# Performance work log

Measured on AMD Instinct MI355X. Metric: run time of the kernel, lower is better.

Reference implementation:

```python
import jax, jax.numpy as jnp
import numpy as np

B, T, TAU = 4, 512, 512
D_MODEL = 1024  # in_dim == out_dim (required: pos embedding dim out_dim feeds pos_proj with in_size=in_dim)
H, D = 16, 64
LN_EPS = 1e-5


def rel_shift(x):
    # x: [B, T, L, H] -> Transformer-XL relative shift
    b, t, l, h = x.shape
    x = jnp.pad(x, ((0, 0), (0, 0), (1, 0), (0, 0)))  # pad j-dim front
    x = x.reshape(b, l + 1, t, h)[:, 1:, :, :]
    return x.reshape(b, t, l, h)


def setup_inputs() -> dict:
    key = jax.random.key(0)
    ks = jax.random.split(key, 7)
    s = 0.02
    return {
        "inputs": jax.random.normal(ks[0], (B, T, D_MODEL), jnp.float32),
        "memory": jax.random.normal(ks[1], (B, TAU, D_MODEL), jnp.float32),
        "w_qkv": jax.random.normal(ks[2], (3 * H * D, D_MODEL), jnp.float32) * s,
        "w_pos": jax.random.normal(ks[3], (H * D, D_MODEL), jnp.float32) * s,
        "w_out": jax.random.normal(ks[4], (D_MODEL, H * D), jnp.float32) * s,
        "uvar": jax.random.normal(ks[5], (H, D), jnp.float32) * s,
        "vvar": jax.random.normal(ks[6], (H, D), jnp.float32) * s,
        "ln_gamma": jnp.ones((D_MODEL,), jnp.float32),
        "ln_beta": jnp.zeros((D_MODEL,), jnp.float32),
    }


def reference(inputs, memory, w_qkv, w_pos, w_out, uvar, vvar, ln_gamma, ln_beta):
    b, t, din = inputs.shape
    tau = memory.shape[1]
    L = tau + t
    h, d = uvar.shape

    x = jnp.concatenate([jax.lax.stop_gradient(memory), inputs], axis=1)  # [B,L,Din]
    # input layernorm
    mu = jnp.mean(x, axis=-1, keepdims=True)
    var = jnp.mean((x - mu) ** 2, axis=-1, keepdims=True)
    x = (x - mu) / jnp.sqrt(var + LN_EPS) * ln_gamma + ln_beta

    qkv = x @ w_qkv.T  # [B,L,3HD]
    q, k, v = jnp.split(qkv, 3, axis=-1)
    q = q[:, -t:].reshape(b, t, h, d)
    k = k.reshape(b, L, h, d)
    v = v.reshape(b, L, h, d)

    # sinusoidal relative position embedding, dim = out_dim (= din here)
    inv_freq = 1.0 / (10000.0 ** (jnp.arange(0, din, 2, dtype=jnp.float32) / din))
    pos = jnp.arange(L - 1, -1, -1, dtype=jnp.float32)
    sin_in = pos[:, None] * inv_freq[None, :]                 # [L, din/2]
    phi = jnp.concatenate([jnp.sin(sin_in), jnp.cos(sin_in)], axis=-1)  # [L, din]
    R = (phi @ w_pos.T).reshape(L, h, d)

    score = jnp.einsum('bihd,bjhd->bijh', q + uvar, k)        # content score
    pos_score = jnp.einsum('bihd,jhd->bijh', q + vvar, R)     # position score
    score = (score + rel_shift(pos_score)) / (d ** 0.5)       # [B,T,L,H]

    # causal mask: query i attends to j <= tau + i
    mask = (jnp.arange(L)[None, :] <= (tau + jnp.arange(t))[:, None]).astype(score.dtype)
    mask = mask[None, :, :, None]
    masked = score * mask + 1e30 * (mask - 1.0)
    w = jax.nn.softmax(masked, axis=2)

    out = jnp.einsum('bijh,bjhd->bihd', w, v).reshape(b, t, h * d)
    return out @ w_out.T
```

## Files before the change

### kernel.cpp

```cpp
#include <hip/hip_runtime.h>
#include <math.h>

#define B_   4
#define T_   512
#define TAU_ 512
#define L_   1024
#define DM_  1024
#define H_   16
#define D_   64

typedef short  s16x8 __attribute__((ext_vector_type(8)));
typedef ushort u16x4 __attribute__((ext_vector_type(4)));
typedef float  f32x4 __attribute__((ext_vector_type(4)));

__device__ __forceinline__ ushort f2bf(float x) {
  uint u = __float_as_uint(x);
  u += 0x7fffu + ((u >> 16) & 1u);
  return (ushort)(u >> 16);
}
__device__ __forceinline__ float bf2f(ushort u) {
  return __uint_as_float(((uint)u) << 16);
}
__device__ __forceinline__ int sw64(int row, int col) {
  return row * 64 + (col ^ ((row & 7) << 3));
}

__global__ __launch_bounds__(256) void prep_kernel(
    const float* __restrict__ inp, const float* __restrict__ mem,
    const float* __restrict__ gamma, const float* __restrict__ beta,
    ushort* __restrict__ xn, ushort* __restrict__ phi,
    const float* __restrict__ wq, ushort* __restrict__ wqb,
    const float* __restrict__ wp, ushort* __restrict__ wpb,
    const float* __restrict__ wo, ushort* __restrict__ wob) {
  int blk = blockIdx.x;
  int t = threadIdx.x;
  if (blk < 4096) {
    int row = blk;
    int b = row >> 10, l = row & 1023;
    const float* src = (l < TAU_)
        ? mem + ((size_t)b * TAU_ + l) * DM_
        : inp + ((size_t)b * T_ + (l - TAU_)) * DM_;
    float4 v = *(const float4*)(src + t * 4);
    float s  = v.x + v.y + v.z + v.w;
    float s2 = v.x * v.x + v.y * v.y + v.z * v.z + v.w * v.w;
#pragma unroll
    for (int off = 32; off > 0; off >>= 1) {
      s  += __shfl_down(s, off);
      s2 += __shfl_down(s2, off);
    }
    __shared__ float red[8];
    __shared__ float stat[2];
    int wid = t >> 6;
    if ((t & 63) == 0) { red[wid * 2] = s; red[wid * 2 + 1] = s2; }
    __syncthreads();
    if (t == 0) {
      float ts  = red[0] + red[2] + red[4] + red[6];
      float ts2 = red[1] + red[3] + red[5] + red[7];
      float mu  = ts * (1.0f / DM_);
      float var = ts2 * (1.0f / DM_) - mu * mu;
      stat[0] = mu;
      stat[1] = 1.0f / sqrtf(var + 1e-5f);
    }
    __syncthreads();
    float mu = stat[0], rstd = stat[1];
    float4 g  = *(const float4*)(gamma + t * 4);
    float4 be = *(const float4*)(beta  + t * 4);
    u16x4 o;
    o[0] = f2bf((v.x - mu) * rstd * g.x + be.x);
    o[1] = f2bf((v.y - mu) * rstd * g.y + be.y);
    o[2] = f2bf((v.z - mu) * rstd * g.z + be.z);
    o[3] = f2bf((v.w - mu) * rstd * g.w + be.w);
    *(u16x4*)(xn + (size_t)row * DM_ + t * 4) = o;
  } else if (blk < 8192) {
    int idx = (blk - 4096) * 256 + t;
    int m = idx >> 10, c = idx & 1023;
    float p = (float)(1023 - m);
    int cc = (c < 512) ? c : c - 512;
    float invf = __expf(-((float)(2 * cc) * (1.0f / 1024.0f)) * 9.210340371976184f);
    float a = p * invf;
    phi[idx] = f2bf((c < 512) ? sinf(a) : cosf(a));
  } else {
    int i = (blk - 8192) * 256 + t;
    const float* src; ushort* dst; int off;
    if (i < 786432)       { src = wq; dst = wqb; off = i; }
    else if (i < 1048576) { src = wp; dst = wpb; off = i - 786432; }
    else                  { src = wo; dst = wob; off = i - 1048576; }
    float4 v = *(const float4*)(src + (size_t)off * 4);
    u16x4 o = { f2bf(v.x), f2bf(v.y), f2bf(v.z), f2bf(v.w) };
    *(u16x4*)(dst + (size_t)off * 4) = o;
  }
}

template <typename CT>
__device__ __forceinline__ void gemm_nt_body(
    const ushort* __restrict__ A, const ushort* __restrict__ B,
    CT* __restrict__ C, int M, int N, int K, int bx, int by) {
  __shared__ __attribute__((aligned(16))) ushort As[128 * 64];
  __shared__ __attribute__((aligned(16))) ushort Bs[128 * 64];
  int t = threadIdx.x;
  int w = t >> 6, lane = t & 63, g = lane >> 4, low = lane & 15;
  int wr = w >> 1, wc = w & 1;
  int m0 = by * 128, n0 = bx * 128;
  f32x4 acc[4][4] = {};

  for (int kt = 0; kt < K; kt += 64) {
    __syncthreads();
#pragma unroll
    for (int q = 0; q < 4; ++q) {
      int c = t + q * 256;
      int row = c >> 3;
      int gslot = (c & 7) ^ (row & 7);
      const ushort* ga = A + (size_t)(m0 + row) * K + kt + gslot * 8;
      const ushort* gb = B + (size_t)(n0 + row) * K + kt + gslot * 8;
      __builtin_amdgcn_global_load_lds(
          (const __attribute__((address_space(1))) void*)ga,
          (__attribute__((address_space(3))) void*)&As[(q * 256 + w * 64) * 8],
          16, 0, 0);
      __builtin_amdgcn_global_load_lds(
          (const __attribute__((address_space(1))) void*)gb,
          (__attribute__((address_space(3))) void*)&Bs[(q * 256 + w * 64) * 8],
          16, 0, 0);
    }
    __syncthreads();

#pragma unroll
    for (int kc = 0; kc < 2; ++kc) {
      s16x8 af[4], bfr[4];
#pragma unroll
      for (int mi = 0; mi < 4; ++mi) {
        int row = wr * 64 + mi * 16 + low;
        af[mi] = *(const s16x8*)&As[row * 64 + (((4 * kc + g) ^ (row & 7)) * 8)];
      }
#pragma unroll
      for (int ni = 0; ni < 4; ++ni) {
        int col = wc * 64 + ni * 16 + low;
        bfr[ni] = *(const s16x8*)&Bs[col * 64 + (((4 * kc + g) ^ (col & 7)) * 8)];
      }
#pragma unroll
      for (int mi = 0; mi < 4; ++mi)
#pragma unroll
        for (int ni = 0; ni < 4; ++ni)
          acc[mi][ni] = __builtin_amdgcn_mfma_f32_16x16x32_bf16(
              af[mi], bfr[ni], acc[mi][ni], 0, 0, 0);
    }
  }
#pragma unroll
  for (int mi = 0; mi < 4; ++mi)
#pragma unroll
    for (int ni = 0; ni < 4; ++ni)
#pragma unroll
      for (int r = 0; r < 4; ++r) {
        int m = m0 + wr * 64 + mi * 16 + 4 * g + r;
        int n = n0 + wc * 64 + ni * 16 + low;
        if constexpr (sizeof(CT) == 2)
          C[(size_t)m * N + n] = f2bf(acc[mi][ni][r]);
        else
          C[(size_t)m * N + n] = acc[mi][ni][r];
      }
}

template <typename CT>
__device__ __forceinline__ void gemm_nt_body_n64(
    const ushort* __restrict__ A, const ushort* __restrict__ B,
    CT* __restrict__ C, int M, int N, int K, int bx, int by) {
  __shared__ __attribute__((aligned(16))) ushort As[128 * 64];
  __shared__ __attribute__((aligned(16))) ushort Bs[64 * 64];
  int t = threadIdx.x;
  int w = t >> 6, lane = t & 63, g = lane >> 4, low = lane & 15;
  int wr = w >> 1, wc = w & 1;
  int m0 = by * 128, n0 = bx * 64;
  f32x4 acc[4][2] = {};

  for (int kt = 0; kt < K; kt += 64) {
    __syncthreads();
#pragma unroll
    for (int q = 0; q < 4; ++q) {
      int c = t + q * 256;
      int row = c >> 3;
      int gslot = (c & 7) ^ (row & 7);
      const ushort* ga = A + (size_t)(m0 + row) * K + kt + gslot * 8;
      __builtin_amdgcn_global_load_lds(
          (const __attribute__((address_space(1))) void*)ga,
          (__attribute__((address_space(3))) void*)&As[(q * 256 + w * 64) * 8],
          16, 0, 0);
    }
#pragma unroll
    for (int q = 0; q < 2; ++q) {
      int c = t + q * 256;
      int row = c >> 3;
      int gslot = (c & 7) ^ (row & 7);
      const ushort* gb = B + (size_t)(n0 + row) * K + kt + gslot * 8;
      __builtin_amdgcn_global_load_lds(
          (const __attribute__((address_space(1))) void*)gb,
          (__attribute__((address_space(3))) void*)&Bs[(q * 256 + w * 64) * 8],
          16, 0, 0);
    }
    __syncthreads();

#pragma unroll
    for (int kc = 0; kc < 2; ++kc) {
      s16x8 af[4], bfr[2];
#pragma unroll
      for (int mi = 0; mi < 4; ++mi) {
        int row = wr * 64 + mi * 16 + low;
        af[mi] = *(const s16x8*)&As[row * 64 + (((4 * kc + g) ^ (row & 7)) * 8)];
      }
#pragma unroll
      for (int ni = 0; ni < 2; ++ni) {
        int col = wc * 32 + ni * 16 + low;
        bfr[ni] = *(const s16x8*)&Bs[col * 64 + (((4 * kc + g) ^ (col & 7)) * 8)];
      }
#pragma unroll
      for (int mi = 0; mi < 4; ++mi)
#pragma unroll
        for (int ni = 0; ni < 2; ++ni)
          acc[mi][ni] = __builtin_amdgcn_mfma_f32_16x16x32_bf16(
              af[mi], bfr[ni], acc[mi][ni], 0, 0, 0);
    }
  }
#pragma unroll
  for (int mi = 0; mi < 4; ++mi)
#pragma unroll
    for (int ni = 0; ni < 2; ++ni)
#pragma unroll
      for (int r = 0; r < 4; ++r) {
        int m = m0 + wr * 64 + mi * 16 + 4 * g + r;
        int n = n0 + wc * 32 + ni * 16 + low;
        if constexpr (sizeof(CT) == 2)
          C[(size_t)m * N + n] = f2bf(acc[mi][ni][r]);
        else
          C[(size_t)m * N + n] = acc[mi][ni][r];
      }
}

__global__ __launch_bounds__(256) void qkv_r_gemm(
    const ushort* __restrict__ xnb, const ushort* __restrict__ wqb,
    ushort* __restrict__ qkvB,
    const ushort* __restrict__ phib, const ushort* __restrict__ wpb,
    ushort* __restrict__ RmB) {
  int orig = blockIdx.x;
  int id = (orig & 7) * 104 + (orig >> 3);
  if (id < 768)
    gemm_nt_body<ushort>(xnb, wqb, qkvB, 4096, 3072, 1024, id % 24, id / 24);
  else {
    id -= 768;
    gemm_nt_body<ushort>(phib, wpb, RmB, 1024, 1024, 1024, id % 8, id / 8);
  }
}

__global__ __launch_bounds__(256) void out_gemm(
    const ushort* __restrict__ attnb, const ushort* __restrict__ wob,
    float* __restrict__ out) {
  int orig = blockIdx.x;
  int id = (orig & 7) * 32 + (orig >> 3);
  gemm_nt_body_n64<float>(attnb, wob, out, 2048, 1024, 1024, id % 16, id / 16);
}

__global__ __launch_bounds__(256) void attn_mfma_kernel(
    const ushort* __restrict__ qkv, const ushort* __restrict__ Rm,
    const float* __restrict__ uvar, const float* __restrict__ vvar,
    ushort* __restrict__ attn) {
  __shared__ __attribute__((aligned(16))) ushort Ks[2][64 * 64];
  __shared__ __attribute__((aligned(16))) ushort Vt[2][64 * 64];
  __shared__ __attribute__((aligned(16))) ushort Rs[2][128 * 64];
  __shared__ __attribute__((aligned(16))) ushort Pp[4][16 * 64];

  int t   = threadIdx.x;
  int w   = t >> 6;
  int lw  = t & 63;
  int g   = lw >> 4;
  int low = lw & 15;

  int bid = blockIdx.x;
  int h   = (bid >> 3) & 15;
  int b   = bid >> 7;
  int bi  = (b >= 2) ? (7 - (bid & 7)) : (bid & 7);
  int i0  = bi * 64;
  int lb_w = 48 - 16 * w;

  auto stage_kr = [&](int buf, int tl) {
    int j0s = tl * 64;
#pragma unroll
    for (int q = 0; q < 2; ++q) {
      int c = t + q * 256;
      int row = c >> 3;
      int sl = (c & 7) ^ (row & 7);
      const ushort* srck = qkv + (size_t)(b * L_ + j0s + row) * 3072 +
                           1024 + h * 64 + sl * 8;
      __builtin_amdgcn_global_load_lds(
          (const __attribute__((address_space(1))) void*)srck,
          (__attribute__((address_space(3))) void*)&Ks[buf][(q * 256 + w * 64) * 8],
          16, 0, 0);
    }
    int mb = j0s + 448 - i0;
#pragma unroll
    for (int q = 0; q < 4; ++q) {
      int c = t + q * 256;
      int row = c >> 3;
      int m = mb + row; m = (m > 1023) ? 1023 : m;
      int sl = (c & 7) ^ (row & 7);
      const ushort* srcr = Rm + (size_t)m * 1024 + h * 64 + sl * 8;
      __builtin_amdgcn_global_load_lds(
          (const __attribute__((address_space(1))) void*)srcr,
          (__attribute__((address_space(3))) void*)&Rs[buf][(q * 256 + w * 64) * 8],
          16, 0, 0);
    }
  };

  int vj  = t & 63;
  int vd0 = (t >> 6) * 8;
  float4 vreg[2];
  auto vload = [&](int tl) {
    const ushort* p = qkv + (size_t)(b * L_ + tl * 64 + vj) * 3072 + 2048 + h * 64;
    vreg[0] = *(const float4*)(p + vd0);
    vreg[1] = *(const float4*)(p + vd0 + 32);
  };
  auto vwrite = [&](int buf) {
#pragma unroll
    for (int it = 0; it < 2; ++it) {
      ushort vals[8];
      *(float4*)vals = vreg[it];
#pragma unroll
      for (int e = 0; e < 8; ++e) {
        int d = it * 32 + vd0 + e;
        Vt[buf][d * 64 + (vj ^ ((d & 7) << 3))] = vals[e];
      }
    }
  };

  int iq = i0 + 16 * w + low;
  s16x8 qu[2], qv[2];
  {
    const ushort* qrow = qkv + (size_t)(b * L_ + TAU_ + iq) * 3072 + h * 64;
    const float* ur = uvar + h * 64;
    const float* vr = vvar + h * 64;
#pragma unroll
    for (int kc = 0; kc < 2; ++kc) {
      int dbase = kc * 32 + 8 * g;
#pragma unroll
      for (int e = 0; e < 8; ++e) {
        float q = bf2f(qrow[dbase + e]);
        qu[kc][e] = (short)f2bf(q + ur[dbase + e]);
        qv[kc][e] = (short)f2bf(q + vr[dbase + e]);
      }
    }
  }

  f32x4 O[4] = {};
  float mreg[4] = {-INFINITY, -INFINITY, -INFINITY, -INFINITY};
  float lreg[4] = {0.f, 0.f, 0.f, 0.f};

  int ntiles = 9 + bi;
  stage_kr(0, 0);
  vload(0);
  vwrite(0);
  __syncthreads();
  int cur = 0;
  for (int tile = 0; tile < ntiles; ++tile) {
    int j0 = tile * 64;
    bool more = (tile + 1 < ntiles);
    if (more) { stage_kr(cur ^ 1, tile + 1); vload(tile + 1); }

    f32x4 s[4] = {};
#pragma unroll
    for (int jt = 0; jt < 4; ++jt) {
#pragma unroll
      for (int kc = 0; kc < 2; ++kc) {
        s16x8 kb = *(const s16x8*)&Ks[cur][sw64(jt * 16 + low, kc * 32 + 8 * g)];
        s[jt] = __builtin_amdgcn_mfma_f32_16x16x32_bf16(qu[kc], kb, s[jt], 0, 0, 0);
      }
    }
    f32x4 p[5] = {};
#pragma unroll
    for (int mt = 0; mt < 5; ++mt) {
#pragma unroll
      for (int kc = 0; kc < 2; ++kc) {
        s16x8 rb = *(const s16x8*)&Rs[cur][sw64(lb_w + mt * 16 + low, kc * 32 + 8 * g)];
        p[mt] = __builtin_amdgcn_mfma_f32_16x16x32_bf16(qv[kc], rb, p[mt], 0, 0, 0);
      }
    }
#pragma unroll
    for (int r = 0; r < 4; ++r) {
      int iL = 4 * g + r;
      int src = g * 16 + ((low + 15 - iL) & 15);
      float sh0 = __shfl(p[0][r], src);
      float sh1 = __shfl(p[1][r], src);
      float sh2 = __shfl(p[2][r], src);
      float sh3 = __shfl(p[3][r], src);
      float sh4 = __shfl(p[4][r], src);
      bool lo = (low <= iL);
      float po0 = lo ? sh0 : sh1;
      float po1 = lo ? sh1 : sh2;
      float po2 = lo ? sh2 : sh3;
      float po3 = lo ? sh3 : sh4;
      int lim = TAU_ + i0 + 16 * w + iL;
      s[0][r] = (j0 +  0 + low <= lim) ? (s[0][r] + po0) * 0.125f : -1e30f;
      s[1][r] = (j0 + 16 + low <= lim) ? (s[1][r] + po1) * 0.125f : -1e30f;
      s[2][r] = (j0 + 32 + low <= lim) ? (s[2][r] + po2) * 0.125f : -1e30f;
      s[3][r] = (j0 + 48 + low <= lim) ? (s[3][r] + po3) * 0.125f : -1e30f;
    }
#pragma unroll
    for (int r = 0; r < 4; ++r) {
      float mx = fmaxf(fmaxf(s[0][r], s[1][r]), fmaxf(s[2][r], s[3][r]));
      mx = fmaxf(mx, __shfl_xor(mx, 1));
      mx = fmaxf(mx, __shfl_xor(mx, 2));
      mx = fmaxf(mx, __shfl_xor(mx, 4));
      mx = fmaxf(mx, __shfl_xor(mx, 8));
      float mn = fmaxf(mreg[r], mx);
      float alpha = __expf(mreg[r] - mn);
      mreg[r] = mn;
      float sum = 0.f;
#pragma unroll
      for (int jt = 0; jt < 4; ++jt) {
        float pe = __expf(s[jt][r] - mn);
        s[jt][r] = pe;
        sum += pe;
      }
      sum += __shfl_xor(sum, 1);
      sum += __shfl_xor(sum, 2);
      sum += __shfl_xor(sum, 4);
      sum += __shfl_xor(sum, 8);
      lreg[r] = lreg[r] * alpha + sum;
      O[0][r] *= alpha; O[1][r] *= alpha; O[2][r] *= alpha; O[3][r] *= alpha;
    }
#pragma unroll
    for (int jt = 0; jt < 4; ++jt)
#pragma unroll
      for (int r = 0; r < 4; ++r)
        Pp[w][sw64(4 * g + r, jt * 16 + low)] = f2bf(s[jt][r]);
    asm volatile("s_waitcnt lgkmcnt(0)" ::: "memory");
    s16x8 pa0 = *(const s16x8*)&Pp[w][sw64(low, 8 * g)];
    s16x8 pa1 = *(const s16x8*)&Pp[w][sw64(low, 32 + 8 * g)];
#pragma unroll
    for (int dt = 0; dt < 4; ++dt) {
      s16x8 v0 = *(const s16x8*)&Vt[cur][sw64(dt * 16 + low, 8 * g)];
      s16x8 v1 = *(const s16x8*)&Vt[cur][sw64(dt * 16 + low, 32 + 8 * g)];
      O[dt] = __builtin_amdgcn_mfma_f32_16x16x32_bf16(pa0, v0, O[dt], 0, 0, 0);
      O[dt] = __builtin_amdgcn_mfma_f32_16x16x32_bf16(pa1, v1, O[dt], 0, 0, 0);
    }
    if (more) vwrite(cur ^ 1);
    __syncthreads();
    cur ^= 1;
  }
  float inv[4];
#pragma unroll
  for (int r = 0; r < 4; ++r) inv[r] = 1.0f / lreg[r];
#pragma unroll
  for (int dt = 0; dt < 4; ++dt)
#pragma unroll
    for (int r = 0; r < 4; ++r)
      attn[((size_t)(b * T_ + i0 + 16 * w + 4 * g + r)) * 1024 +
           h * 64 + dt * 16 + low] = f2bf(O[dt][r] * inv[r]);
}

extern "C" void kernel_launch(void* const* d_in, const int* in_sizes, int n_in,
                              void* d_out, int out_size, void* d_ws, size_t ws_size,
                              hipStream_t stream) {
  const float* inputs = (const float*)d_in[0];
  const float* memory = (const float*)d_in[1];
  const float* w_qkv  = (const float*)d_in[2];
  const float* w_pos  = (const float*)d_in[3];
  const float* w_out  = (const float*)d_in[4];
  const float* uvar   = (const float*)d_in[5];
  const float* vvar   = (const float*)d_in[6];
  const float* gamma  = (const float*)d_in[7];
  const float* beta   = (const float*)d_in[8];
  float* out = (float*)d_out;

  ushort* qkvB = (ushort*)d_ws;
  ushort* xnb  = qkvB + (size_t)4096 * 3072;
  ushort* phib = xnb  + (size_t)4096 * 1024;
  ushort* RmB  = phib + (size_t)1024 * 1024;
  ushort* wqb  = RmB  + (size_t)1024 * 1024;
  ushort* wpb  = wqb  + (size_t)3072 * 1024;
  ushort* wob  = wpb  + (size_t)1024 * 1024;
  ushort* attnb = xnb;

  prep_kernel<<<13312, 256, 0, stream>>>(inputs, memory, gamma, beta, xnb,
                                         phib, w_qkv, wqb, w_pos, wpb, w_out, wob);
  qkv_r_gemm<<<832, 256, 0, stream>>>(xnb, wqb, qkvB, phib, wpb, RmB);
  attn_mfma_kernel<<<dim3(B_ * H_ * 8), 256, 0, stream>>>(qkvB, RmB, uvar, vvar, attnb);
  out_gemm<<<256, 256, 0, stream>>>(attnb, wob, out);
}
```

Measured before the change: 209.1 us.

## Double-buffer GEMM LDS tiles with K=32 stages and use fast sin/cos

The two NT GEMM bodies now use two LDS buffers of K=32 slices and prefetch the next slice via global_load_lds while MFMAs run on the current one. This cuts the barrier count per iteration from two to one and is meant to overlap global loads with compute. The swizzle changes to fit 32-wide rows. The position embedding also switches to the __sinf/__cosf intrinsics, which lose accuracy for large arguments (positions up to 1023). The smaller K slice doubles the loop iterations and barrier frequency.

```diff
diff --git a/kernel.cpp b/kernel.cpp
--- a/kernel.cpp
+++ b/kernel.cpp
@@ -78,7 +78,7 @@
     int cc = (c < 512) ? c : c - 512;
     float invf = __expf(-((float)(2 * cc) * (1.0f / 1024.0f)) * 9.210340371976184f);
     float a = p * invf;
-    phi[idx] = f2bf((c < 512) ? sinf(a) : cosf(a));
+    phi[idx] = f2bf((c < 512) ? __sinf(a) : __cosf(a));
   } else {
     int i = (blk - 8192) * 256 + t;
     const float* src; ushort* dst; int off;
@@ -95,54 +95,58 @@
 __device__ __forceinline__ void gemm_nt_body(
     const ushort* __restrict__ A, const ushort* __restrict__ B,
     CT* __restrict__ C, int M, int N, int K, int bx, int by) {
-  __shared__ __attribute__((aligned(16))) ushort As[128 * 64];
-  __shared__ __attribute__((aligned(16))) ushort Bs[128 * 64];
+  __shared__ __attribute__((aligned(16))) ushort As[2][128 * 32];
+  __shared__ __attribute__((aligned(16))) ushort Bs[2][128 * 32];
   int t = threadIdx.x;
   int w = t >> 6, lane = t & 63, g = lane >> 4, low = lane & 15;
   int wr = w >> 1, wc = w & 1;
   int m0 = by * 128, n0 = bx * 128;
   f32x4 acc[4][4] = {};
 
-  for (int kt = 0; kt < K; kt += 64) {
-    __syncthreads();
-#pragma unroll
-    for (int q = 0; q < 4; ++q) {
-      int c = t + q * 256;
-      int row = c >> 3;
-      int gslot = (c & 7) ^ (row & 7);
+  auto stage = [&](int buf, int kt) {
+#pragma unroll
+    for (int q = 0; q < 2; ++q) {
+      int f = t + q * 256;
+      int row = f >> 2;
+      int gslot = (f & 3) ^ ((row >> 1) & 3);
       const ushort* ga = A + (size_t)(m0 + row) * K + kt + gslot * 8;
       const ushort* gb = B + (size_t)(n0 + row) * K + kt + gslot * 8;
       __builtin_amdgcn_global_load_lds(
           (const __attribute__((address_space(1))) void*)ga,
-          (__attribute__((address_space(3))) void*)&As[(q * 256 + w * 64) * 8],
+          (__attribute__((address_space(3))) void*)&As[buf][(q * 256 + w * 64) * 8],
           16, 0, 0);
       __builtin_amdgcn_global_load_lds(
           (const __attribute__((address_space(1))) void*)gb,
-          (__attribute__((address_space(3))) void*)&Bs[(q * 256 + w * 64) * 8],
-          16, 0, 0);
-    }
+          (__attribute__((address_space(3))) void*)&Bs[buf][(q * 256 + w * 64) * 8],
+          16, 0, 0);
+    }
+  };
+
+  stage(0, 0);
+  __syncthreads();
+  int cur = 0;
+  for (int kt = 0; kt < K; kt += 32) {
+    if (kt + 32 < K) stage(cur ^ 1, kt + 32);
+
+    s16x8 af[4], bfr[4];
+#pragma unroll
+    for (int mi = 0; mi < 4; ++mi) {
+      int row = wr * 64 + mi * 16 + low;
+      af[mi] = *(const s16x8*)&As[cur][row * 32 + ((g ^ ((row >> 1) & 3)) * 8)];
+    }
+#pragma unroll
+    for (int ni = 0; ni < 4; ++ni) {
+      int col = wc * 64 + ni * 16 + low;
+      bfr[ni] = *(const s16x8*)&Bs[cur][col * 32 + ((g ^ ((col >> 1) & 3)) * 8)];
+    }
+#pragma unroll
+    for (int mi = 0; mi < 4; ++mi)
+#pragma unroll
+      for (int ni = 0; ni < 4; ++ni)
+        acc[mi][ni] = __builtin_amdgcn_mfma_f32_16x16x32_bf16(
+            af[mi], bfr[ni], acc[mi][ni], 0, 0, 0);
     __syncthreads();
-
-#pragma unroll
-    for (int kc = 0; kc < 2; ++kc) {
-      s16x8 af[4], bfr[4];
-#pragma unroll
-      for (int mi = 0; mi < 4; ++mi) {
-        int row = wr * 64 + mi * 16 + low;
-        af[mi] = *(const s16x8*)&As[row * 64 + (((4 * kc + g) ^ (row & 7)) * 8)];
-      }
-#pragma unroll
-      for (int ni = 0; ni < 4; ++ni) {
-        int col = wc * 64 + ni * 16 + low;
-        bfr[ni] = *(const s16x8*)&Bs[col * 64 + (((4 * kc + g) ^ (col & 7)) * 8)];
-      }
-#pragma unroll
-      for (int mi = 0; mi < 4; ++mi)
-#pragma unroll
-        for (int ni = 0; ni < 4; ++ni)
-          acc[mi][ni] = __builtin_amdgcn_mfma_f32_16x16x32_bf16(
-              af[mi], bfr[ni], acc[mi][ni], 0, 0, 0);
-    }
+    cur ^= 1;
   }
 #pragma unroll
   for (int mi = 0; mi < 4; ++mi)
@@ -163,60 +167,63 @@
 __device__ __forceinline__ void gemm_nt_body_n64(
     const ushort* __restrict__ A, const ushort* __restrict__ B,
     CT* __restrict__ C, int M, int N, int K, int bx, int by) {
-  __shared__ __attribute__((aligned(16))) ushort As[128 * 64];
-  __shared__ __attribute__((aligned(16))) ushort Bs[64 * 64];
+  __shared__ __attribute__((aligned(16))) ushort As[2][128 * 32];
+  __shared__ __attribute__((aligned(16))) ushort Bs[2][64 * 32];
   int t = threadIdx.x;
   int w = t >> 6, lane = t & 63, g = lane >> 4, low = lane & 15;
   int wr = w >> 1, wc = w & 1;
   int m0 = by * 128, n0 = bx * 64;
   f32x4 acc[4][2] = {};
 
-  for (int kt = 0; kt < K; kt += 64) {
+  auto stage = [&](int buf, int kt) {
+#pragma unroll
+    for (int q = 0; q < 2; ++q) {
+      int f = t + q * 256;
+      int row = f >> 2;
+      int gslot = (f & 3) ^ ((row >> 1) & 3);
+      const ushort* ga = A + (size_t)(m0 + row) * K + kt + gslot * 8;
+      __builtin_amdgcn_global_load_lds(
+          (const __attribute__((address_space(1))) void*)ga,
+          (__attribute__((address_space(3))) void*)&As[buf][(q * 256 + w * 64) * 8],
+          16, 0, 0);
+    }
+    {
+      int f = t;
+      int row = f >> 2;
+      int gslot = (f & 3) ^ ((row >> 1) & 3);
+      const ushort* gb = B + (size_t)(n0 + row) * K + kt + gslot * 8;
+      __builtin_amdgcn_global_load_lds(
+          (const __attribute__((address_space(1))) void*)gb,
+          (__attribute__((address_space(3))) void*)&Bs[buf][(w * 64) * 8],
+          16, 0, 0);
+    }
+  };
+
+  stage(0, 0);
+  __syncthreads();
+  int cur = 0;
+  for (int kt = 0; kt < K; kt += 32) {
+    if (kt + 32 < K) stage(cur ^ 1, kt + 32);
+
+    s16x8 af[4], bfr[2];
+#pragma unroll
+    for (int mi = 0; mi < 4; ++mi) {
+      int row = wr * 64 + mi * 16 + low;
+      af[mi] = *(const s16x8*)&As[cur][row * 32 + ((g ^ ((row >> 1) & 3)) * 8)];
+    }
+#pragma unroll
+    for (int ni = 0; ni < 2; ++ni) {
+      int col = wc * 32 + ni * 16 + low;
+      bfr[ni] = *(const s16x8*)&Bs[cur][col * 32 + ((g ^ ((col >> 1) & 3)) * 8)];
+    }
+#pragma unroll
+    for (int mi = 0; mi < 4; ++mi)
+#pragma unroll
+      for (int ni = 0; ni < 2; ++ni)
+        acc[mi][ni] = __builtin_amdgcn_mfma_f32_16x16x32_bf16(
+            af[mi], bfr[ni], acc[mi][ni], 0, 0, 0);
     __syncthreads();
-#pragma unroll
-    for (int q = 0; q < 4; ++q) {
-      int c = t + q * 256;
-      int row = c >> 3;
-      int gslot = (c & 7) ^ (row & 7);
-      const ushort* ga = A + (size_t)(m0 + row) * K + kt + gslot * 8;
-      __builtin_amdgcn_global_load_lds(
-          (const __attribute__((address_space(1))) void*)ga,
-          (__attribute__((address_space(3))) void*)&As[(q * 256 + w * 64) * 8],
-          16, 0, 0);
-    }
-#pragma unroll
-    for (int q = 0; q < 2; ++q) {
-      int c = t + q * 256;
-      int row = c >> 3;
-      int gslot = (c & 7) ^ (row & 7);
-      const ushort* gb = B + (size_t)(n0 + row) * K + kt + gslot * 8;
-      __builtin_amdgcn_global_load_lds(
-          (const __attribute__((address_space(1))) void*)gb,
-          (__attribute__((address_space(3))) void*)&Bs[(q * 256 + w * 64) * 8],
-          16, 0, 0);
-    }
-    __syncthreads();
-
-#pragma unroll
-    for (int kc = 0; kc < 2; ++kc) {
-      s16x8 af[4], bfr[2];
-#pragma unroll
-      for (int mi = 0; mi < 4; ++mi) {
-        int row = wr * 64 + mi * 16 + low;
-        af[mi] = *(const s16x8*)&As[row * 64 + (((4 * kc + g) ^ (row & 7)) * 8)];
-      }
-#pragma unroll
-      for (int ni = 0; ni < 2; ++ni) {
-        int col = wc * 32 + ni * 16 + low;
-        bfr[ni] = *(const s16x8*)&Bs[col * 64 + (((4 * kc + g) ^ (col & 7)) * 8)];
-      }
-#pragma unroll
-      for (int mi = 0; mi < 4; ++mi)
-#pragma unroll
-        for (int ni = 0; ni < 2; ++ni)
-          acc[mi][ni] = __builtin_amdgcn_mfma_f32_16x16x32_bf16(
-              af[mi], bfr[ni], acc[mi][ni], 0, 0, 0);
-    }
+    cur ^= 1;
   }
 #pragma unroll
   for (int mi = 0; mi < 4; ++mi)
```

After: 212.4 us. About the same (+1.5%).

## Coarsen prep kernel to wave-per-row LayerNorm and rebalance attention block order

Applied to the files above, without the earlier changes.

The prep kernel now gives each wave one LayerNorm row, reducing with shuffles only, so the shared-memory reductions and block barriers are gone. The phi and weight-conversion branches each handle four elements per thread, and phi uses the fast __sinf/__cosf intrinsics, which cuts the prep grid to a quarter of its old size. The attention kernel remaps block IDs so consecutive blocks alternate short and long causal row tiles and spread across heads and batches, aiming for better load balance across CUs. The fast sin/cos intrinsics lose accuracy for large arguments (up to about 1023), which could slightly change the bf16 position embeddings.

```diff
diff --git a/kernel.cpp b/kernel.cpp
--- a/kernel.cpp
+++ b/kernel.cpp
@@ -34,60 +34,65 @@
     const float* __restrict__ wo, ushort* __restrict__ wob) {
   int blk = blockIdx.x;
   int t = threadIdx.x;
-  if (blk < 4096) {
-    int row = blk;
+  if (blk < 1024) {
+    int wid = t >> 6, lane = t & 63;
+    int row = blk * 4 + wid;
     int b = row >> 10, l = row & 1023;
     const float* src = (l < TAU_)
         ? mem + ((size_t)b * TAU_ + l) * DM_
         : inp + ((size_t)b * T_ + (l - TAU_)) * DM_;
-    float4 v = *(const float4*)(src + t * 4);
-    float s  = v.x + v.y + v.z + v.w;
-    float s2 = v.x * v.x + v.y * v.y + v.z * v.z + v.w * v.w;
+    float4 v[4];
+    float s1 = 0.f, s2 = 0.f;
+#pragma unroll
+    for (int c = 0; c < 4; ++c) {
+      v[c] = *(const float4*)(src + c * 256 + lane * 4);
+      s1 += v[c].x + v[c].y + v[c].z + v[c].w;
+      s2 += v[c].x * v[c].x + v[c].y * v[c].y + v[c].z * v[c].z + v[c].w * v[c].w;
+    }
 #pragma unroll
     for (int off = 32; off > 0; off >>= 1) {
-      s  += __shfl_down(s, off);
-      s2 += __shfl_down(s2, off);
-    }
-    __shared__ float red[8];
-    __shared__ float stat[2];
-    int wid = t >> 6;
-    if ((t & 63) == 0) { red[wid * 2] = s; red[wid * 2 + 1] = s2; }
-    __syncthreads();
-    if (t == 0) {
-      float ts  = red[0] + red[2] + red[4] + red[6];
-      float ts2 = red[1] + red[3] + red[5] + red[7];
-      float mu  = ts * (1.0f / DM_);
-      float var = ts2 * (1.0f / DM_) - mu * mu;
-      stat[0] = mu;
-      stat[1] = 1.0f / sqrtf(var + 1e-5f);
-    }
-    __syncthreads();
-    float mu = stat[0], rstd = stat[1];
-    float4 g  = *(const float4*)(gamma + t * 4);
-    float4 be = *(const float4*)(beta  + t * 4);
-    u16x4 o;
-    o[0] = f2bf((v.x - mu) * rstd * g.x + be.x);
-    o[1] = f2bf((v.y - mu) * rstd * g.y + be.y);
-    o[2] = f2bf((v.z - mu) * rstd * g.z + be.z);
-    o[3] = f2bf((v.w - mu) * rstd * g.w + be.w);
-    *(u16x4*)(xn + (size_t)row * DM_ + t * 4) = o;
-  } else if (blk < 8192) {
-    int idx = (blk - 4096) * 256 + t;
-    int m = idx >> 10, c = idx & 1023;
-    float p = (float)(1023 - m);
-    int cc = (c < 512) ? c : c - 512;
-    float invf = __expf(-((float)(2 * cc) * (1.0f / 1024.0f)) * 9.210340371976184f);
-    float a = p * invf;
-    phi[idx] = f2bf((c < 512) ? sinf(a) : cosf(a));
+      s1 += __shfl_xor(s1, off);
+      s2 += __shfl_xor(s2, off);
+    }
+    float mu   = s1 * (1.0f / DM_);
+    float var  = s2 * (1.0f / DM_) - mu * mu;
+    float rstd = 1.0f / sqrtf(var + 1e-5f);
+#pragma unroll
+    for (int c = 0; c < 4; ++c) {
+      float4 g  = *(const float4*)(gamma + c * 256 + lane * 4);
+      float4 be = *(const float4*)(beta  + c * 256 + lane * 4);
+      u16x4 o;
+      o[0] = f2bf((v[c].x - mu) * rstd * g.x + be.x);
+      o[1] = f2bf((v[c].y - mu) * rstd * g.y + be.y);
+      o[2] = f2bf((v[c].z - mu) * rstd * g.z + be.z);
+      o[3] = f2bf((v[c].w - mu) * rstd * g.w + be.w);
+      *(u16x4*)(xn + (size_t)row * DM_ + c * 256 + lane * 4) = o;
+    }
+  } else if (blk < 2048) {
+    int base = (blk - 1024) * 1024 + t;
+#pragma unroll
+    for (int it = 0; it < 4; ++it) {
+      int idx = base + it * 256;
+      int m = idx >> 10, c = idx & 1023;
+      float p = (float)(1023 - m);
+      int cc = (c < 512) ? c : c - 512;
+      float invf = __expf(-((float)(2 * cc) * (1.0f / 1024.0f)) * 9.210340371976184f);
+      float a = p * invf;
+      phi[idx] = f2bf((c < 512) ? __sinf(a) : __cosf(a));
+    }
   } else {
-    int i = (blk - 8192) * 256 + t;
-    const float* src; ushort* dst; int off;
-    if (i < 786432)       { src = wq; dst = wqb; off = i; }
-    else if (i < 1048576) { src = wp; dst = wpb; off = i - 786432; }
-    else                  { src = wo; dst = wob; off = i - 1048576; }
-    float4 v = *(const float4*)(src + (size_t)off * 4);
-    u16x4 o = { f2bf(v.x), f2bf(v.y), f2bf(v.z), f2bf(v.w) };
-    *(u16x4*)(dst + (size_t)off * 4) = o;
+    int base = (blk - 2048) * 1024 + t;
+#pragma unroll
+    for (int it = 0; it < 4; ++it) {
+      int i = base + it * 256;
+      const float* src; ushort* dst; int off;
+      if (i < 786432)       { src = wq; dst = wqb; off = i; }
+      else if (i < 1048576) { src = wp; dst = wpb; off = i - 786432; }
+      else                  { src = wo; dst = wob; off = i - 1048576; }
+      float4 v = *(const float4*)(src + (size_t)off * 4);
+      u16x4 o = { f2bf(v.x), f2bf(v.y), f2bf(v.z), f2bf(v.w) };
+      *(u16x4*)(dst + (size_t)off * 4) = o;
+    }
   }
 }
 
@@ -271,11 +276,13 @@
   int g   = lw >> 4;
   int low = lw & 15;
 
-  int bid = blockIdx.x;
-  int h   = (bid >> 3) & 15;
-  int b   = bid >> 7;
-  int bi  = (b >= 2) ? (7 - (bid & 7)) : (bid & 7);
-  int i0  = bi * 64;
+  int orig = blockIdx.x;
+  int bid  = (orig & 7) * 64 + (orig >> 3);
+  int s    = bid & 7;
+  int h    = (bid >> 3) & 15;
+  int b    = bid >> 7;
+  int bi   = (s & 1) ? (7 - (s >> 1)) : (s >> 1);
+  int i0   = bi * 64;
   int lb_w = 48 - 16 * w;
 
   auto stage_kr = [&](int buf, int tl) {
@@ -361,13 +368,13 @@
     bool more = (tile + 1 < ntiles);
     if (more) { stage_kr(cur ^ 1, tile + 1); vload(tile + 1); }
 
-    f32x4 s[4] = {};
+    f32x4 s4[4] = {};
 #pragma unroll
     for (int jt = 0; jt < 4; ++jt) {
 #pragma unroll
       for (int kc = 0; kc < 2; ++kc) {
         s16x8 kb = *(const s16x8*)&Ks[cur][sw64(jt * 16 + low, kc * 32 + 8 * g)];
-        s[jt] = __builtin_amdgcn_mfma_f32_16x16x32_bf16(qu[kc], kb, s[jt], 0, 0, 0);
+        s4[jt] = __builtin_amdgcn_mfma_f32_16x16x32_bf16(qu[kc], kb, s4[jt], 0, 0, 0);
       }
     }
     f32x4 p[5] = {};
@@ -394,14 +401,14 @@
       float po2 = lo ? sh2 : sh3;
       float po3 = lo ? sh3 : sh4;
       int lim = TAU_ + i0 + 16 * w + iL;
-      s[0][r] = (j0 +  0 + low <= lim) ? (s[0][r] + po0) * 0.125f : -1e30f;
-      s[1][r] = (j0 + 16 + low <= lim) ? (s[1][r] + po1) * 0.125f : -1e30f;
-      s[2][r] = (j0 + 32 + low <= lim) ? (s[2][r] + po2) * 0.125f : -1e30f;
-      s[3][r] = (j0 + 48 + low <= lim) ? (s[3][r] + po3) * 0.125f : -1e30f;
+      s4[0][r] = (j0 +  0 + low <= lim) ? (s4[0][r] + po0) * 0.125f : -1e30f;
+      s4[1][r] = (j0 + 16 + low <= lim) ? (s4[1][r] + po1) * 0.125f : -1e30f;
+      s4[2][r] = (j0 + 32 + low <= lim) ? (s4[2][r] + po2) * 0.125f : -1e30f;
+      s4[3][r] = (j0 + 48 + low <= lim) ? (s4[3][r] + po3) * 0.125f : -1e30f;
     }
 #pragma unroll
     for (int r = 0; r < 4; ++r) {
-      float mx = fmaxf(fmaxf(s[0][r], s[1][r]), fmaxf(s[2][r], s[3][r]));
+      float mx = fmaxf(fmaxf(s4[0][r], s4[1][r]), fmaxf(s4[2][r], s4[3][r]));
       mx = fmaxf(mx, __shfl_xor(mx, 1));
       mx = fmaxf(mx, __shfl_xor(mx, 2));
       mx = fmaxf(mx, __shfl_xor(mx, 4));
@@ -412,8 +419,8 @@
       float sum = 0.f;
 #pragma unroll
       for (int jt = 0; jt < 4; ++jt) {
-        float pe = __expf(s[jt][r] - mn);
-        s[jt][r] = pe;
+        float pe = __expf(s4[jt][r] - mn);
+        s4[jt][r] = pe;
         sum += pe;
       }
       sum += __shfl_xor(sum, 1);
@@ -427,7 +434,7 @@
     for (int jt = 0; jt < 4; ++jt)
 #pragma unroll
       for (int r = 0; r < 4; ++r)
-        Pp[w][sw64(4 * g + r, jt * 16 + low)] = f2bf(s[jt][r]);
+        Pp[w][sw64(4 * g + r, jt * 16 + low)] = f2bf(s4[jt][r]);
     asm volatile("s_waitcnt lgkmcnt(0)" ::: "memory");
     s16x8 pa0 = *(const s16x8*)&Pp[w][sw64(low, 8 * g)];
     s16x8 pa1 = *(const s16x8*)&Pp[w][sw64(low, 32 + 8 * g)];
@@ -476,8 +483,8 @@
   ushort* wob  = wpb  + (size_t)1024 * 1024;
   ushort* attnb = xnb;
 
-  prep_kernel<<<13312, 256, 0, stream>>>(inputs, memory, gamma, beta, xnb,
-                                         phib, w_qkv, wqb, w_pos, wpb, w_out, wob);
+  prep_kernel<<<3328, 256, 0, stream>>>(inputs, memory, gamma, beta, xnb,
+                                        phib, w_qkv, wqb, w_pos, wpb, w_out, wob);
   qkv_r_gemm<<<832, 256, 0, stream>>>(xnb, wqb, qkvB, phib, wpb, RmB);
   attn_mfma_kernel<<<dim3(B_ * H_ * 8), 256, 0, stream>>>(qkvB, RmB, uvar, vvar, attnb);
   out_gemm<<<256, 256, 0, stream>>>(attnb, wob, out);
```

New measurement: 203.1 us. 2.9% less time.
